# Optimization experiments

Hardware: AMD Instinct MI355X
Metric: run time of the kernel (lower is better)

The kernel has to match this reference:

```python
import jax, jax.numpy as jnp
import numpy as np

B, S, N, D, H = 4, 2048, 2048, 1024, 16
HD = D // H  # 64
EPS = 1e-5


def layer_norm(x, w, b):
    m = x.mean(axis=-1, keepdims=True)
    v = ((x - m) ** 2).mean(axis=-1, keepdims=True)
    return (x - m) / jnp.sqrt(v + EPS) * w + b


def setup_inputs() -> dict:
    key = jax.random.key(0)
    ks = jax.random.split(key, 4)
    x_q = jax.random.normal(ks[0], (B, S, D), dtype=jnp.float32)
    x_k = jax.random.normal(ks[1], (B, N, HD), dtype=jnp.float32)
    x_v = jax.random.normal(ks[2], (B, N, HD), dtype=jnp.float32)
    # learned params
    qn_w = jnp.ones((HD,), jnp.float32)
    qn_b = jnp.zeros((HD,), jnp.float32)
    kn_w = jnp.ones((HD,), jnp.float32)
    kn_b = jnp.zeros((HD,), jnp.float32)
    n_w = jnp.ones((D,), jnp.float32)
    n_b = jnp.zeros((D,), jnp.float32)
    # xavier-uniform proj weight (D, D), no bias (proj_bias=False)
    limit = np.sqrt(6.0 / (D + D))
    proj_w = jax.random.uniform(ks[3], (D, D), jnp.float32, -limit, limit)
    return {"x_q": x_q, "x_k": x_k, "x_v": x_v,
            "qn_w": qn_w, "qn_b": qn_b, "kn_w": kn_w, "kn_b": kn_b,
            "n_w": n_w, "n_b": n_b, "proj_w": proj_w}


def reference(x_q, x_k, x_v, qn_w, qn_b, kn_w, kn_b, n_w, n_b, proj_w):
    scale = HD ** -0.5
    # faithful to torch: q.reshape(B, H, -1, head_dim) -- NO transpose before reshape
    q = x_q.reshape(B, H, S, HD)
    q = layer_norm(q, qn_w, qn_b)
    k = layer_norm(x_k, kn_w, kn_b)
    q = q * scale
    attn = jnp.einsum('bhsd,bnd->bhsn', q, k)  # (B,H,S,N) shared K across heads
    attn = jax.nn.softmax(attn, axis=-1)
    x = jnp.einsum('bhsn,bnd->bhsd', attn, x_v)  # shared V across heads
    x = jnp.transpose(x, (0, 2, 1, 3)).reshape(B, S, D)
    x = layer_norm(x, n_w, n_b)
    x = x @ proj_w.T  # nn.Linear: x W^T
    return x
```

## Files before the change

kernel.cpp:

```cpp
#include <hip/hip_runtime.h>

#define B_ 4
#define S_ 2048
#define N_ 2048
#define H_ 16
#define D_ 1024

typedef short s4v __attribute__((ext_vector_type(4)));
typedef short s8v __attribute__((ext_vector_type(8)));
typedef float f4v __attribute__((ext_vector_type(4)));
typedef float f2v __attribute__((ext_vector_type(2)));

__device__ __forceinline__ float bf2f(short s) {
  unsigned u = ((unsigned)(unsigned short)s) << 16;
  float f; __builtin_memcpy(&f, &u, 4); return f;
}
__device__ __forceinline__ short f2bf(float f) {
  unsigned u; __builtin_memcpy(&u, &f, 4);
  u += 0x7fffu + ((u >> 16) & 1u);
  return (short)(u >> 16);
}
__device__ __forceinline__ unsigned pack2bf(float a, float b) {
  unsigned ua, ub;
  __builtin_memcpy(&ua, &a, 4);
  __builtin_memcpy(&ub, &b, 4);
  return __builtin_amdgcn_perm(ub + 0x8000u, ua + 0x8000u, 0x07060302u);
}
__device__ __forceinline__ unsigned pk2(float a, float b) {
  unsigned ua, ub;
  __builtin_memcpy(&ua, &a, 4);
  __builtin_memcpy(&ub, &b, 4);
  return __builtin_amdgcn_perm(ub, ua, 0x07060302u);
}
__device__ __forceinline__ s8v load8f32(const float* p) {
  const f4v* q = (const f4v*)p;
  f4v a = q[0], b = q[1];
  union { s8v v; unsigned u[4]; } o;
  o.u[0] = pack2bf(a[0], a[1]); o.u[1] = pack2bf(a[2], a[3]);
  o.u[2] = pack2bf(b[0], b[1]); o.u[3] = pack2bf(b[2], b[3]);
  return o.v;
}
__device__ __forceinline__ void gld16(const char* g, char* l) {
  __builtin_amdgcn_global_load_lds(
      (const __attribute__((address_space(1))) unsigned*)g,
      (__attribute__((address_space(3))) unsigned*)l, 16, 0, 0);
}

__global__ __launch_bounds__(256) void prep_kernel(
    const float* __restrict__ xk, const float* __restrict__ knw,
    const float* __restrict__ knb, short* __restrict__ kws,
    const float* __restrict__ xv, short* __restrict__ vtp,
    const float* __restrict__ pw, const float* __restrict__ nw_,
    const float* __restrict__ nb_, short* __restrict__ wpb,
    float* __restrict__ t12) {
  __shared__ __align__(16) short vstage[4][2048];
  int blk = blockIdx.x;
  if (blk < 2048) {
    int gid = blk * 256 + threadIdx.x;
    int row = gid >> 6, lane = gid & 63;
    float v = xk[(size_t)row * 64 + lane];
    float s = v;
    #pragma unroll
    for (int mm = 1; mm < 64; mm <<= 1) s += __shfl_xor(s, mm, 64);
    float mean = s * 0.015625f;
    float d = v - mean;
    float vs = d * d;
    #pragma unroll
    for (int mm = 1; mm < 64; mm <<= 1) vs += __shfl_xor(vs, mm, 64);
    float rstd = rsqrtf(vs * 0.015625f + 1e-5f);
    kws[(size_t)row * 72 + lane] = f2bf(d * rstd * knw[lane] + knb[lane]);
  } else if (blk < 2112) {
    int wave = threadIdx.x >> 6, lane = threadIdx.x & 63;
    int u = (blk - 2048) * 4 + wave;
    int b = u >> 6, nb = u & 63;
    int r = lane >> 1, dh = lane & 1;
    const float* src = xv + ((size_t)(b * N_ + nb * 32 + r)) * 64 + dh * 32;
    int qq = (r & 15) >> 2;
    int slot = ((r >> 4) << 2) + (r & 3);
    short* wbase = &vstage[wave][0];
    #pragma unroll
    for (int jj = 0; jj < 32; jj += 4) {
      f4v f = *(const f4v*)(src + jj);
      #pragma unroll
      for (int e = 0; e < 4; e++) {
        int d = dh * 32 + jj + e;
        wbase[d * 32 + qq * 8 + slot] = f2bf(f[e]);
      }
    }
    __syncthreads();
    s8v* dst = (s8v*)(vtp + (size_t)u * 2560 + lane * 40);
    const s8v* sp = (const s8v*)(wbase + lane * 32);
    dst[0] = sp[0]; dst[1] = sp[1]; dst[2] = sp[2]; dst[3] = sp[3];
  } else {
    int jr = threadIdx.x >> 4;
    int lc = (threadIdx.x & 15) * 64;
    int j = (blk - 2112) * 16 + jr;
    const float* wr = pw + (size_t)j * 1024 + lc;
    float t1p = 0.f, t2p = 0.f;
    #pragma unroll
    for (int c = 0; c < 64; c += 8) {
      f4v w0 = *(const f4v*)(wr + c);
      f4v w1 = *(const f4v*)(wr + c + 4);
      f4v g0 = *(const f4v*)(nw_ + lc + c);
      f4v g1 = *(const f4v*)(nw_ + lc + c + 4);
      f4v b0 = *(const f4v*)(nb_ + lc + c);
      f4v b1 = *(const f4v*)(nb_ + lc + c + 4);
      float p[8];
      #pragma unroll
      for (int e = 0; e < 4; e++) {
        p[e]     = g0[e] * w0[e];
        p[4 + e] = g1[e] * w1[e];
        t1p += p[e] + p[4 + e];
        t2p += b0[e] * w0[e] + b1[e] * w1[e];
      }
      union { s8v v; unsigned u[4]; } o8;
      o8.u[0] = pack2bf(p[0], p[1]); o8.u[1] = pack2bf(p[2], p[3]);
      o8.u[2] = pack2bf(p[4], p[5]); o8.u[3] = pack2bf(p[6], p[7]);
      *(s8v*)(wpb + (size_t)j * 1024 + lc + c) = o8.v;
    }
    #pragma unroll
    for (int mm = 1; mm < 16; mm <<= 1) {
      t1p += __shfl_xor(t1p, mm, 64);
      t2p += __shfl_xor(t2p, mm, 64);
    }
    if ((threadIdx.x & 15) == 0) { t12[j * 2] = t1p; t12[j * 2 + 1] = t2p; }
  }
}

__global__ __launch_bounds__(256, 4) void flash_kernel(
    const float* __restrict__ xq, const float* __restrict__ qnw,
    const float* __restrict__ qnb, const short* __restrict__ kws,
    const short* __restrict__ vtp, short* __restrict__ aout,
    float* __restrict__ stp) {
  __shared__ __align__(16) union {
    char qs[128 * 144];
    struct { char k[2][9216]; char v[2][10240]; } kv;
  } lds;
  int blk = blockIdx.x;
  int sblk = blk & 15, bh = blk >> 4, b = bh >> 4;
  int t = threadIdx.x, wave = t >> 6, lane = t & 63;
  int m = lane & 15, q = lane >> 4;
  const float QSCALE = 0.125f * 1.4426950408889634f;

  const char* kb = (const char*)kws + (size_t)b * N_ * 144;
  const char* vb = (const char*)vtp + (size_t)b * 64 * 5120;

  gld16(vb + t * 16,        lds.kv.v[0] + t * 16);
  gld16(vb + 4096 + t * 16, lds.kv.v[0] + 4096 + t * 16);
  if (t < 128) gld16(vb + 8192 + t * 16, lds.kv.v[0] + 8192 + t * 16);

  {
    int r = t >> 1, half = t & 1;
    const float* qr = xq + ((size_t)bh * S_ + sblk * 128 + r) * 64 + half * 32;
    f4v f[8];
    float s = 0.f, ss = 0.f;
    #pragma unroll
    for (int i = 0; i < 8; i++) {
      f[i] = *(const f4v*)(qr + i * 4);
      s += (f[i][0] + f[i][1]) + (f[i][2] + f[i][3]);
      ss += (f[i][0] * f[i][0] + f[i][1] * f[i][1]) + (f[i][2] * f[i][2] + f[i][3] * f[i][3]);
    }
    s += __shfl_xor(s, 1, 64);
    ss += __shfl_xor(ss, 1, 64);
    float mean = s * 0.015625f;
    float rstd = rsqrtf(ss * 0.015625f - mean * mean + 1e-5f);
    #pragma unroll
    for (int i = 0; i < 4; i++) {
      float y[8];
      #pragma unroll
      for (int e = 0; e < 4; e++) {
        int gi = half * 32 + i * 8;
        y[e]     = ((f[2 * i][e]     - mean) * rstd * qnw[gi + e]     + qnb[gi + e])     * QSCALE;
        y[4 + e] = ((f[2 * i + 1][e] - mean) * rstd * qnw[gi + 4 + e] + qnb[gi + 4 + e]) * QSCALE;
      }
      union { s8v v; unsigned u[4]; } o8;
      #pragma unroll
      for (int e = 0; e < 4; e++) o8.u[e] = pack2bf(y[2 * e], y[2 * e + 1]);
      *(s8v*)(lds.qs + r * 144 + half * 64 + i * 16) = o8.v;
    }
  }
  __syncthreads();

  s8v qlo[2], qhi[2];
  #pragma unroll
  for (int mt = 0; mt < 2; mt++) {
    const char* qrow = lds.qs + (wave * 32 + mt * 16 + m) * 144;
    qlo[mt] = *(const s8v*)(qrow + q * 16);
    qhi[mt] = *(const s8v*)(qrow + 64 + q * 16);
  }
  __syncthreads();

  gld16(kb + t * 16,        lds.kv.k[0] + t * 16);
  gld16(kb + 4096 + t * 16, lds.kv.k[0] + 4096 + t * 16);
  if (t < 64) gld16(kb + 8192 + t * 16, lds.kv.k[0] + 8192 + t * 16);
  __syncthreads();

  f4v zero4 = {0.f, 0.f, 0.f, 0.f};
  f4v o[2][4], lacc[2];
  #pragma unroll
  for (int mt = 0; mt < 2; mt++) {
    lacc[mt] = zero4;
    #pragma unroll
    for (int tt = 0; tt < 4; tt++) o[mt][tt] = zero4;
  }
  s8v ones;
  #pragma unroll
  for (int e = 0; e < 8; e++) ones[e] = (short)0x3F80;

  for (int it = 0; it < 32; ++it) {
    int cur = it & 1;
    if (it < 31) {
      const char* kg = kb + (size_t)(it + 1) * 9216;
      const char* vg = vb + (size_t)(it + 1) * 10240;
      char* kd = lds.kv.k[cur ^ 1];
      char* vd = lds.kv.v[cur ^ 1];
      gld16(kg + t * 16,        kd + t * 16);
      gld16(kg + 4096 + t * 16, kd + 4096 + t * 16);
      if (t < 64) gld16(kg + 8192 + t * 16, kd + 8192 + t * 16);
      gld16(vg + t * 16,        vd + t * 16);
      gld16(vg + 4096 + t * 16, vd + 4096 + t * 16);
      if (t < 128) gld16(vg + 8192 + t * 16, vd + 8192 + t * 16);
    }
    const char* kc = lds.kv.k[cur];
    const char* vc = lds.kv.v[cur];

    #pragma unroll
    for (int g = 0; g < 2; g++) {
      s8v a0lo = *(const s8v*)(kc + (g * 32 + m) * 144 + q * 16);
      s8v a0hi = *(const s8v*)(kc + (g * 32 + m) * 144 + 64 + q * 16);
      s8v a1lo = *(const s8v*)(kc + (g * 32 + 16 + m) * 144 + q * 16);
      s8v a1hi = *(const s8v*)(kc + (g * 32 + 16 + m) * 144 + 64 + q * 16);
      s8v vf[4];
      #pragma unroll
      for (int tt = 0; tt < 4; tt++)
        vf[tt] = *(const s8v*)(vc + g * 5120 + (tt * 16 + m) * 80 + q * 16);

      #pragma unroll
      for (int mt = 0; mt < 2; mt++) {
        f4v s0 = zero4, s1 = zero4;
        s0 = __builtin_amdgcn_mfma_f32_16x16x32_bf16(a0lo, qlo[mt], s0, 0, 0, 0);
        s0 = __builtin_amdgcn_mfma_f32_16x16x32_bf16(a0hi, qhi[mt], s0, 0, 0, 0);
        s1 = __builtin_amdgcn_mfma_f32_16x16x32_bf16(a1lo, qlo[mt], s1, 0, 0, 0);
        s1 = __builtin_amdgcn_mfma_f32_16x16x32_bf16(a1hi, qhi[mt], s1, 0, 0, 0);
        float p[8];
        #pragma unroll
        for (int i = 0; i < 4; i++) {
          p[i]     = __builtin_amdgcn_exp2f(s0[i]);
          p[4 + i] = __builtin_amdgcn_exp2f(s1[i]);
        }
        union { s8v v; unsigned u[4]; } pa;
        #pragma unroll
        for (int i = 0; i < 4; i++) pa.u[i] = pk2(p[2 * i], p[2 * i + 1]);
        lacc[mt] = __builtin_amdgcn_mfma_f32_16x16x32_bf16(pa.v, ones, lacc[mt], 0, 0, 0);
        #pragma unroll
        for (int tt = 0; tt < 4; tt++)
          o[mt][tt] = __builtin_amdgcn_mfma_f32_16x16x32_bf16(pa.v, vf[tt], o[mt][tt], 0, 0, 0);
      }
    }
    __syncthreads();
  }

  int head = bh & 15;
  #pragma unroll
  for (int mt = 0; mt < 2; mt++) {
    #pragma unroll
    for (int i = 0; i < 4; i++) {
      float inv = __builtin_amdgcn_rcpf(lacc[mt][i]);
      int srow = sblk * 128 + wave * 32 + mt * 16 + q * 4 + i;
      size_t orow = ((size_t)b * S_ + srow) * D_ + (size_t)head * 64;
      float ps = 0.f, pss = 0.f;
      #pragma unroll
      for (int tt = 0; tt < 4; tt++) {
        float v = o[mt][tt][i] * inv;
        ps += v; pss += v * v;
        aout[orow + tt * 16 + m] = f2bf(v);
      }
      #pragma unroll
      for (int mm = 1; mm < 16; mm <<= 1) {
        ps += __shfl_xor(ps, mm, 64);
        pss += __shfl_xor(pss, mm, 64);
      }
      if (m == 0) {
        size_t gr = (size_t)b * S_ + srow;
        f2v pv = {ps, pss};
        *(f2v*)(stp + (gr * 16 + head) * 2) = pv;
      }
    }
  }
}

__global__ __launch_bounds__(256) void ln_d_kernel(
    const short* __restrict__ x, const float* __restrict__ w,
    const float* __restrict__ bb, short* __restrict__ y) {
  int row = blockIdx.x * 4 + (threadIdx.x >> 6);
  int lane = threadIdx.x & 63;
  const short* xr = x + (size_t)row * D_ + lane * 16;
  s8v v0 = *(const s8v*)xr;
  s8v v1 = *(const s8v*)(xr + 8);
  float f[16];
  #pragma unroll
  for (int e = 0; e < 8; e++) { f[e] = bf2f(v0[e]); f[8 + e] = bf2f(v1[e]); }
  float s = 0.f, ss = 0.f;
  #pragma unroll
  for (int e = 0; e < 16; e++) { s += f[e]; ss += f[e] * f[e]; }
  #pragma unroll
  for (int mm = 1; mm < 64; mm <<= 1) {
    s += __shfl_xor(s, mm, 64);
    ss += __shfl_xor(ss, mm, 64);
  }
  float mean = s * (1.0f / 1024.0f);
  float rstd = rsqrtf(ss * (1.0f / 1024.0f) - mean * mean + 1e-5f);
  const float* wp = w + lane * 16;
  const float* bp = bb + lane * 16;
  union { s8v v[2]; short sh[16]; } o;
  #pragma unroll
  for (int e = 0; e < 16; e++)
    o.sh[e] = f2bf((f[e] - mean) * rstd * wp[e] + bp[e]);
  short* yr = y + (size_t)row * D_ + lane * 16;
  *(s8v*)yr = o.v[0];
  *(s8v*)(yr + 8) = o.v[1];
}

__global__ __launch_bounds__(256, 2) void proj_gemm_fb(
    const short* __restrict__ A, const float* __restrict__ Bw,
    float* __restrict__ C) {
  __shared__ __align__(16) char la[2][16384];
  __shared__ __align__(16) char lb[2][16384];
  int wg = (blockIdx.x & 7) * 64 + (blockIdx.x >> 3);
  int bm = (wg >> 3) * 128;
  int bn = (wg & 7) * 128;
  int t = threadIdx.x, wave = t >> 6, lane = t & 63;
  int m = lane & 15, q = lane >> 4;
  int wm = (wave & 1) * 64, wn = (wave >> 1) * 64;

  int arow0 = t >> 3, au = t & 7;
  const char* abase = (const char*)(A + (size_t)bm * 1024);
  int brow = t >> 1, bu0 = (t & 1) * 4;
  const float* bwbase = Bw + (size_t)(bn + brow) * 1024;
  char* lbrow0 = lb[0] + brow * 128;
  char* lbrow1 = lb[1] + brow * 128;

  f4v zero4 = {0.f, 0.f, 0.f, 0.f};
  f4v acc[4][4];
  #pragma unroll
  for (int i = 0; i < 4; i++)
    #pragma unroll
    for (int j = 0; j < 4; j++) acc[i][j] = zero4;

  #pragma unroll
  for (int c = 0; c < 4; c++) {
    int row = c * 32 + arow0;
    gld16(abase + (size_t)row * 2048 + (size_t)(au ^ (row & 7)) * 16,
          la[0] + c * 4096 + t * 16);
  }
  #pragma unroll
  for (int j = 0; j < 4; j++) {
    int u = bu0 + j;
    s8v bv = load8f32(bwbase + u * 8);
    *(s8v*)(lbrow0 + ((u ^ (brow & 7)) * 16)) = bv;
  }
  __syncthreads();

  for (int it = 0; it < 16; ++it) {
    int cur = it & 1;
    if (it < 15) {
      int k0 = (it + 1) * 64;
      char* ad = la[cur ^ 1];
      char* bd = (cur ^ 1) ? lbrow1 : lbrow0;
      #pragma unroll
      for (int c = 0; c < 4; c++) {
        int row = c * 32 + arow0;
        gld16(abase + (size_t)row * 2048 + (size_t)k0 * 2 +
                  (size_t)(au ^ (row & 7)) * 16,
              ad + c * 4096 + t * 16);
      }
      #pragma unroll
      for (int j = 0; j < 4; j++) {
        int u = bu0 + j;
        s8v bv = load8f32(bwbase + k0 + u * 8);
        *(s8v*)(bd + ((u ^ (brow & 7)) * 16)) = bv;
      }
    }
    const char* lac = la[cur];
    const char* lbc = lb[cur];
    #pragma unroll
    for (int kh = 0; kh < 2; kh++) {
      s8v af[4], bfv[4];
      #pragma unroll
      for (int i = 0; i < 4; i++) {
        int r = wm + i * 16 + m;
        af[i] = *(const s8v*)(lac + r * 128 + (((kh * 4 + q) ^ (r & 7)) * 16));
      }
      #pragma unroll
      for (int j = 0; j < 4; j++) {
        int r = wn + j * 16 + m;
        bfv[j] = *(const s8v*)(lbc + r * 128 + (((kh * 4 + q) ^ (r & 7)) * 16));
      }
      #pragma unroll
      for (int i = 0; i < 4; i++)
        #pragma unroll
        for (int j = 0; j < 4; j++)
          acc[i][j] = __builtin_amdgcn_mfma_f32_16x16x32_bf16(af[i], bfv[j], acc[i][j], 0, 0, 0);
    }
    __syncthreads();
  }

  #pragma unroll
  for (int i = 0; i < 4; i++)
    #pragma unroll
    for (int j = 0; j < 4; j++)
      #pragma unroll
      for (int r = 0; r < 4; r++) {
        int row = bm + wm + i * 16 + q * 4 + r;
        int col = bn + wn + j * 16 + m;
        C[(size_t)row * 1024 + col] = acc[i][j][r];
      }
}

__global__ __launch_bounds__(256, 2) void proj_gemm_fx(
    const short* __restrict__ A, const short* __restrict__ Wp,
    const float* __restrict__ t12, const float* __restrict__ stp,
    float* __restrict__ C) {
  __shared__ __align__(16) char la[2][16384];
  __shared__ __align__(16) char lb[2][16384];
  int wg = (blockIdx.x & 7) * 64 + (blockIdx.x >> 3);
  int bm = (wg >> 3) * 128;
  int bn = (wg & 7) * 128;
  int t = threadIdx.x, wave = t >> 6, lane = t & 63;
  int m = lane & 15, q = lane >> 4;
  int wm = (wave & 1) * 64, wn = (wave >> 1) * 64;

  int arow0 = t >> 3, au = t & 7;
  const char* abase = (const char*)(A + (size_t)bm * 1024);
  const char* bbase = (const char*)(Wp + (size_t)bn * 1024);

  f4v zero4 = {0.f, 0.f, 0.f, 0.f};
  f4v acc[4][4];
  #pragma unroll
  for (int i = 0; i < 4; i++)
    #pragma unroll
    for (int j = 0; j < 4; j++) acc[i][j] = zero4;

  #pragma unroll
  for (int c = 0; c < 4; c++) {
    int row = c * 32 + arow0;
    size_t so = (size_t)row * 2048 + (size_t)(au ^ (row & 7)) * 16;
    gld16(abase + so, la[0] + c * 4096 + t * 16);
    gld16(bbase + so, lb[0] + c * 4096 + t * 16);
  }
  __syncthreads();

  for (int it = 0; it < 16; ++it) {
    int cur = it & 1;
    if (it < 15) {
      int k0 = (it + 1) * 64;
      #pragma unroll
      for (int c = 0; c < 4; c++) {
        int row = c * 32 + arow0;
        size_t so = (size_t)row * 2048 + (size_t)k0 * 2 +
                    (size_t)(au ^ (row & 7)) * 16;
        gld16(abase + so, la[cur ^ 1] + c * 4096 + t * 16);
        gld16(bbase + so, lb[cur ^ 1] + c * 4096 + t * 16);
      }
    }
    const char* lac = la[cur];
    const char* lbc = lb[cur];
    #pragma unroll
    for (int kh = 0; kh < 2; kh++) {
      s8v af[4], bfv[4];
      #pragma unroll
      for (int i = 0; i < 4; i++) {
        int r = wm + i * 16 + m;
        af[i] = *(const s8v*)(lac + r * 128 + (((kh * 4 + q) ^ (r & 7)) * 16));
      }
      #pragma unroll
      for (int j = 0; j < 4; j++) {
        int r = wn + j * 16 + m;
        bfv[j] = *(const s8v*)(lbc + r * 128 + (((kh * 4 + q) ^ (r & 7)) * 16));
      }
      #pragma unroll
      for (int i = 0; i < 4; i++)
        #pragma unroll
        for (int j = 0; j < 4; j++)
          acc[i][j] = __builtin_amdgcn_mfma_f32_16x16x32_bf16(af[i], bfv[j], acc[i][j], 0, 0, 0);
    }
    __syncthreads();
  }

  f2v tc[4];
  #pragma unroll
  for (int j = 0; j < 4; j++)
    tc[j] = *(const f2v*)(t12 + (size_t)(bn + wn + j * 16 + m) * 2);
  #pragma unroll
  for (int i = 0; i < 4; i++)
    #pragma unroll
    for (int r = 0; r < 4; r++) {
      int row = bm + wm + i * 16 + q * 4 + r;
      f2v pp = *(const f2v*)(stp + ((size_t)row * 16 + m) * 2);
      float s_ = pp[0], ss_ = pp[1];
      #pragma unroll
      for (int mm = 1; mm < 16; mm <<= 1) {
        s_ += __shfl_xor(s_, mm, 64);
        ss_ += __shfl_xor(ss_, mm, 64);
      }
      float mean = s_ * (1.0f / 1024.0f);
      float rstd = rsqrtf(ss_ * (1.0f / 1024.0f) - mean * mean + 1e-5f);
      float mrs = -mean * rstd;
      #pragma unroll
      for (int j = 0; j < 4; j++) {
        int col = bn + wn + j * 16 + m;
        C[(size_t)row * 1024 + col] =
            rstd * acc[i][j][r] + mrs * tc[j][0] + tc[j][1];
      }
    }
}

extern "C" void kernel_launch(void* const* d_in, const int* in_sizes, int n_in,
                              void* d_out, int out_size, void* d_ws, size_t ws_size,
                              hipStream_t stream) {
  const float* xq  = (const float*)d_in[0];
  const float* xk  = (const float*)d_in[1];
  const float* xv  = (const float*)d_in[2];
  const float* qnw = (const float*)d_in[3];
  const float* qnb = (const float*)d_in[4];
  const float* knw = (const float*)d_in[5];
  const float* knb = (const float*)d_in[6];
  const float* nw  = (const float*)d_in[7];
  const float* nb  = (const float*)d_in[8];
  const float* pw  = (const float*)d_in[9];
  float* out = (float*)d_out;

  const size_t NEED = 22421504;
  if (ws_size >= NEED) {
    short* aoutw = (short*)d_ws;
    short* kws = (short*)((char*)d_ws + 16777216);
    short* vtp = (short*)((char*)d_ws + 17956864);
    short* wpb = (short*)((char*)d_ws + 19267584);
    float* t12 = (float*)((char*)d_ws + 21364736);
    float* stp = (float*)((char*)d_ws + 21372928);
    prep_kernel<<<2176, 256, 0, stream>>>(xk, knw, knb, kws, xv, vtp,
                                          pw, nw, nb, wpb, t12);
    flash_kernel<<<1024, 256, 0, stream>>>(xq, qnw, qnb, kws, vtp, aoutw, stp);
    proj_gemm_fx<<<512, 256, 0, stream>>>(aoutw, wpb, t12, stp, out);
  } else {
    short* kws = (short*)d_ws;
    short* vtp = (short*)((char*)d_ws + 0x120000);
    short* yws = (short*)d_ws;
    short* aout = (short*)d_out;
    float* stdummy = (float*)((char*)d_out + 20971520);
    prep_kernel<<<2112, 256, 0, stream>>>(xk, knw, knb, kws, xv, vtp,
                                          pw, nw, nb, (short*)d_ws, (float*)d_ws);
    flash_kernel<<<1024, 256, 0, stream>>>(xq, qnw, qnb, kws, vtp, aout, stdummy);
    ln_d_kernel<<<B_ * S_ / 4, 256, 0, stream>>>(aout, nw, nb, yws);
    proj_gemm_fb<<<512, 256, 0, stream>>>(yws, pw, out);
  }
}
```

Before: 199.6 us.

## Halve flash-attention tile to 64 queries and 32 keys per step for occupancy

The flash kernel now handles 64 query rows per block (16 per wave) instead of 128, and 32 keys per iteration instead of 64. LDS use and accumulator registers are halved, launch bounds go to 8 blocks per CU, and the grid doubles to 2048 blocks. The aim is more resident waves to hide the latency of exp, MFMA and LDS loads. In exchange, each K/V tile is reused by fewer queries, so global and LDS traffic per FLOP doubles, and there are twice as many barriers per key.

```diff
diff --git a/kernel.cpp b/kernel.cpp
--- a/kernel.cpp
+++ b/kernel.cpp
@@ -127,17 +127,17 @@
   }
 }
 
-__global__ __launch_bounds__(256, 4) void flash_kernel(
+__global__ __launch_bounds__(256, 8) void flash_kernel(
     const float* __restrict__ xq, const float* __restrict__ qnw,
     const float* __restrict__ qnb, const short* __restrict__ kws,
     const short* __restrict__ vtp, short* __restrict__ aout,
     float* __restrict__ stp) {
   __shared__ __align__(16) union {
-    char qs[128 * 144];
-    struct { char k[2][9216]; char v[2][10240]; } kv;
+    char qs[64 * 144];
+    struct { char k[2][4608]; char v[2][5120]; } kv;
   } lds;
   int blk = blockIdx.x;
-  int sblk = blk & 15, bh = blk >> 4, b = bh >> 4;
+  int sblk = blk & 31, bh = blk >> 5, b = bh >> 4;
   int t = threadIdx.x, wave = t >> 6, lane = t & 63;
   int m = lane & 15, q = lane >> 4;
   const float QSCALE = 0.125f * 1.4426950408889634f;
@@ -145,146 +145,129 @@
   const char* kb = (const char*)kws + (size_t)b * N_ * 144;
   const char* vb = (const char*)vtp + (size_t)b * 64 * 5120;
 
-  gld16(vb + t * 16,        lds.kv.v[0] + t * 16);
-  gld16(vb + 4096 + t * 16, lds.kv.v[0] + 4096 + t * 16);
-  if (t < 128) gld16(vb + 8192 + t * 16, lds.kv.v[0] + 8192 + t * 16);
+  gld16(vb + t * 16, lds.kv.v[0] + t * 16);
+  if (t < 64) gld16(vb + (256 + t) * 16, lds.kv.v[0] + (256 + t) * 16);
 
   {
-    int r = t >> 1, half = t & 1;
-    const float* qr = xq + ((size_t)bh * S_ + sblk * 128 + r) * 64 + half * 32;
-    f4v f[8];
+    int r = t >> 2, c4 = t & 3;
+    const float* qr = xq + ((size_t)bh * S_ + sblk * 64 + r) * 64 + c4 * 16;
+    f4v f[4];
     float s = 0.f, ss = 0.f;
     #pragma unroll
-    for (int i = 0; i < 8; i++) {
+    for (int i = 0; i < 4; i++) {
       f[i] = *(const f4v*)(qr + i * 4);
       s += (f[i][0] + f[i][1]) + (f[i][2] + f[i][3]);
       ss += (f[i][0] * f[i][0] + f[i][1] * f[i][1]) + (f[i][2] * f[i][2] + f[i][3] * f[i][3]);
     }
-    s += __shfl_xor(s, 1, 64);
-    ss += __shfl_xor(ss, 1, 64);
+    s += __shfl_xor(s, 1, 64);  ss += __shfl_xor(ss, 1, 64);
+    s += __shfl_xor(s, 2, 64);  ss += __shfl_xor(ss, 2, 64);
     float mean = s * 0.015625f;
     float rstd = rsqrtf(ss * 0.015625f - mean * mean + 1e-5f);
     #pragma unroll
-    for (int i = 0; i < 4; i++) {
+    for (int i = 0; i < 2; i++) {
       float y[8];
       #pragma unroll
       for (int e = 0; e < 4; e++) {
-        int gi = half * 32 + i * 8;
+        int gi = c4 * 16 + i * 8;
         y[e]     = ((f[2 * i][e]     - mean) * rstd * qnw[gi + e]     + qnb[gi + e])     * QSCALE;
         y[4 + e] = ((f[2 * i + 1][e] - mean) * rstd * qnw[gi + 4 + e] + qnb[gi + 4 + e]) * QSCALE;
       }
       union { s8v v; unsigned u[4]; } o8;
       #pragma unroll
       for (int e = 0; e < 4; e++) o8.u[e] = pack2bf(y[2 * e], y[2 * e + 1]);
-      *(s8v*)(lds.qs + r * 144 + half * 64 + i * 16) = o8.v;
+      *(s8v*)(lds.qs + r * 144 + c4 * 32 + i * 16) = o8.v;
     }
   }
   __syncthreads();
 
-  s8v qlo[2], qhi[2];
-  #pragma unroll
-  for (int mt = 0; mt < 2; mt++) {
-    const char* qrow = lds.qs + (wave * 32 + mt * 16 + m) * 144;
-    qlo[mt] = *(const s8v*)(qrow + q * 16);
-    qhi[mt] = *(const s8v*)(qrow + 64 + q * 16);
+  s8v qlo, qhi;
+  {
+    const char* qrow = lds.qs + (wave * 16 + m) * 144;
+    qlo = *(const s8v*)(qrow + q * 16);
+    qhi = *(const s8v*)(qrow + 64 + q * 16);
   }
   __syncthreads();
 
-  gld16(kb + t * 16,        lds.kv.k[0] + t * 16);
-  gld16(kb + 4096 + t * 16, lds.kv.k[0] + 4096 + t * 16);
-  if (t < 64) gld16(kb + 8192 + t * 16, lds.kv.k[0] + 8192 + t * 16);
+  gld16(kb + t * 16, lds.kv.k[0] + t * 16);
+  if (t < 32) gld16(kb + (256 + t) * 16, lds.kv.k[0] + (256 + t) * 16);
   __syncthreads();
 
   f4v zero4 = {0.f, 0.f, 0.f, 0.f};
-  f4v o[2][4], lacc[2];
-  #pragma unroll
-  for (int mt = 0; mt < 2; mt++) {
-    lacc[mt] = zero4;
-    #pragma unroll
-    for (int tt = 0; tt < 4; tt++) o[mt][tt] = zero4;
-  }
+  f4v o[4], lacc = zero4;
+  #pragma unroll
+  for (int tt = 0; tt < 4; tt++) o[tt] = zero4;
   s8v ones;
   #pragma unroll
   for (int e = 0; e < 8; e++) ones[e] = (short)0x3F80;
 
-  for (int it = 0; it < 32; ++it) {
+  for (int it = 0; it < 64; ++it) {
     int cur = it & 1;
-    if (it < 31) {
-      const char* kg = kb + (size_t)(it + 1) * 9216;
-      const char* vg = vb + (size_t)(it + 1) * 10240;
+    if (it < 63) {
+      const char* kg = kb + (size_t)(it + 1) * 4608;
+      const char* vg = vb + (size_t)(it + 1) * 5120;
       char* kd = lds.kv.k[cur ^ 1];
       char* vd = lds.kv.v[cur ^ 1];
-      gld16(kg + t * 16,        kd + t * 16);
-      gld16(kg + 4096 + t * 16, kd + 4096 + t * 16);
-      if (t < 64) gld16(kg + 8192 + t * 16, kd + 8192 + t * 16);
-      gld16(vg + t * 16,        vd + t * 16);
-      gld16(vg + 4096 + t * 16, vd + 4096 + t * 16);
-      if (t < 128) gld16(vg + 8192 + t * 16, vd + 8192 + t * 16);
+      gld16(kg + t * 16, kd + t * 16);
+      if (t >= 128 && t < 160) gld16(kg + (128 + t) * 16, kd + (128 + t) * 16);
+      gld16(vg + t * 16, vd + t * 16);
+      if (t >= 192) gld16(vg + (64 + t) * 16, vd + (64 + t) * 16);
     }
     const char* kc = lds.kv.k[cur];
     const char* vc = lds.kv.v[cur];
 
-    #pragma unroll
-    for (int g = 0; g < 2; g++) {
-      s8v a0lo = *(const s8v*)(kc + (g * 32 + m) * 144 + q * 16);
-      s8v a0hi = *(const s8v*)(kc + (g * 32 + m) * 144 + 64 + q * 16);
-      s8v a1lo = *(const s8v*)(kc + (g * 32 + 16 + m) * 144 + q * 16);
-      s8v a1hi = *(const s8v*)(kc + (g * 32 + 16 + m) * 144 + 64 + q * 16);
-      s8v vf[4];
-      #pragma unroll
-      for (int tt = 0; tt < 4; tt++)
-        vf[tt] = *(const s8v*)(vc + g * 5120 + (tt * 16 + m) * 80 + q * 16);
-
-      #pragma unroll
-      for (int mt = 0; mt < 2; mt++) {
-        f4v s0 = zero4, s1 = zero4;
-        s0 = __builtin_amdgcn_mfma_f32_16x16x32_bf16(a0lo, qlo[mt], s0, 0, 0, 0);
-        s0 = __builtin_amdgcn_mfma_f32_16x16x32_bf16(a0hi, qhi[mt], s0, 0, 0, 0);
-        s1 = __builtin_amdgcn_mfma_f32_16x16x32_bf16(a1lo, qlo[mt], s1, 0, 0, 0);
-        s1 = __builtin_amdgcn_mfma_f32_16x16x32_bf16(a1hi, qhi[mt], s1, 0, 0, 0);
-        float p[8];
-        #pragma unroll
-        for (int i = 0; i < 4; i++) {
-          p[i]     = __builtin_amdgcn_exp2f(s0[i]);
-          p[4 + i] = __builtin_amdgcn_exp2f(s1[i]);
-        }
-        union { s8v v; unsigned u[4]; } pa;
-        #pragma unroll
-        for (int i = 0; i < 4; i++) pa.u[i] = pk2(p[2 * i], p[2 * i + 1]);
-        lacc[mt] = __builtin_amdgcn_mfma_f32_16x16x32_bf16(pa.v, ones, lacc[mt], 0, 0, 0);
-        #pragma unroll
-        for (int tt = 0; tt < 4; tt++)
-          o[mt][tt] = __builtin_amdgcn_mfma_f32_16x16x32_bf16(pa.v, vf[tt], o[mt][tt], 0, 0, 0);
-      }
-    }
+    s8v a0lo = *(const s8v*)(kc + m * 144 + q * 16);
+    s8v a0hi = *(const s8v*)(kc + m * 144 + 64 + q * 16);
+    s8v a1lo = *(const s8v*)(kc + (16 + m) * 144 + q * 16);
+    s8v a1hi = *(const s8v*)(kc + (16 + m) * 144 + 64 + q * 16);
+    s8v vf[4];
+    #pragma unroll
+    for (int tt = 0; tt < 4; tt++)
+      vf[tt] = *(const s8v*)(vc + (tt * 16 + m) * 80 + q * 16);
+
+    f4v s0 = zero4, s1 = zero4;
+    s0 = __builtin_amdgcn_mfma_f32_16x16x32_bf16(a0lo, qlo, s0, 0, 0, 0);
+    s0 = __builtin_amdgcn_mfma_f32_16x16x32_bf16(a0hi, qhi, s0, 0, 0, 0);
+    s1 = __builtin_amdgcn_mfma_f32_16x16x32_bf16(a1lo, qlo, s1, 0, 0, 0);
+    s1 = __builtin_amdgcn_mfma_f32_16x16x32_bf16(a1hi, qhi, s1, 0, 0, 0);
+    float p[8];
+    #pragma unroll
+    for (int i = 0; i < 4; i++) {
+      p[i]     = __builtin_amdgcn_exp2f(s0[i]);
+      p[4 + i] = __builtin_amdgcn_exp2f(s1[i]);
+    }
+    union { s8v v; unsigned u[4]; } pa;
+    #pragma unroll
+    for (int i = 0; i < 4; i++) pa.u[i] = pk2(p[2 * i], p[2 * i + 1]);
+    lacc = __builtin_amdgcn_mfma_f32_16x16x32_bf16(pa.v, ones, lacc, 0, 0, 0);
+    #pragma unroll
+    for (int tt = 0; tt < 4; tt++)
+      o[tt] = __builtin_amdgcn_mfma_f32_16x16x32_bf16(pa.v, vf[tt], o[tt], 0, 0, 0);
+
     __syncthreads();
   }
 
   int head = bh & 15;
   #pragma unroll
-  for (int mt = 0; mt < 2; mt++) {
-    #pragma unroll
-    for (int i = 0; i < 4; i++) {
-      float inv = __builtin_amdgcn_rcpf(lacc[mt][i]);
-      int srow = sblk * 128 + wave * 32 + mt * 16 + q * 4 + i;
-      size_t orow = ((size_t)b * S_ + srow) * D_ + (size_t)head * 64;
-      float ps = 0.f, pss = 0.f;
-      #pragma unroll
-      for (int tt = 0; tt < 4; tt++) {
-        float v = o[mt][tt][i] * inv;
-        ps += v; pss += v * v;
-        aout[orow + tt * 16 + m] = f2bf(v);
-      }
-      #pragma unroll
-      for (int mm = 1; mm < 16; mm <<= 1) {
-        ps += __shfl_xor(ps, mm, 64);
-        pss += __shfl_xor(pss, mm, 64);
-      }
-      if (m == 0) {
-        size_t gr = (size_t)b * S_ + srow;
-        f2v pv = {ps, pss};
-        *(f2v*)(stp + (gr * 16 + head) * 2) = pv;
-      }
+  for (int i = 0; i < 4; i++) {
+    float inv = __builtin_amdgcn_rcpf(lacc[i]);
+    int srow = sblk * 64 + wave * 16 + q * 4 + i;
+    size_t orow = ((size_t)b * S_ + srow) * D_ + (size_t)head * 64;
+    float ps = 0.f, pss = 0.f;
+    #pragma unroll
+    for (int tt = 0; tt < 4; tt++) {
+      float v = o[tt][i] * inv;
+      ps += v; pss += v * v;
+      aout[orow + tt * 16 + m] = f2bf(v);
+    }
+    #pragma unroll
+    for (int mm = 1; mm < 16; mm <<= 1) {
+      ps += __shfl_xor(ps, mm, 64);
+      pss += __shfl_xor(pss, mm, 64);
+    }
+    if (m == 0) {
+      size_t gr = (size_t)b * S_ + srow;
+      f2v pv = {ps, pss};
+      *(f2v*)(stp + (gr * 16 + head) * 2) = pv;
     }
   }
 }
@@ -540,7 +523,7 @@
     float* stp = (float*)((char*)d_ws + 21372928);
     prep_kernel<<<2176, 256, 0, stream>>>(xk, knw, knb, kws, xv, vtp,
                                           pw, nw, nb, wpb, t12);
-    flash_kernel<<<1024, 256, 0, stream>>>(xq, qnw, qnb, kws, vtp, aoutw, stp);
+    flash_kernel<<<2048, 256, 0, stream>>>(xq, qnw, qnb, kws, vtp, aoutw, stp);
     proj_gemm_fx<<<512, 256, 0, stream>>>(aoutw, wpb, t12, stp, out);
   } else {
     short* kws = (short*)d_ws;
@@ -550,7 +533,7 @@
     float* stdummy = (float*)((char*)d_out + 20971520);
     prep_kernel<<<2112, 256, 0, stream>>>(xk, knw, knb, kws, xv, vtp,
                                           pw, nw, nb, (short*)d_ws, (float*)d_ws);
-    flash_kernel<<<1024, 256, 0, stream>>>(xq, qnw, qnb, kws, vtp, aout, stdummy);
+    flash_kernel<<<2048, 256, 0, stream>>>(xq, qnw, qnb, kws, vtp, aout, stdummy);
     ln_d_kernel<<<B_ * S_ / 4, 256, 0, stream>>>(aout, nw, nb, yws);
     proj_gemm_fb<<<512, 256, 0, stream>>>(yws, pw, out);
   }
```

Result: slower. 218.2 us (+9.3%).
